# Kernel tuning notes

Hardware: AMD Instinct MI355X
Metric: run time of the kernel (lower is better)

Reference implementation:

```python
import jax, jax.numpy as jnp
import numpy as np

PAD_ID = 0


def setup_inputs() -> dict:
    key = jax.random.key(0)
    ks = jax.random.split(key, 12)
    B, T, A, E, H, V = 32, 512, 512, 256, 320, 8192
    s = 0.02
    emb = jax.random.normal(ks[0], (V, E), jnp.float32) * s
    emb = emb.at[PAD_ID].set(0.0)  # padding_idx row is zero
    return {
        "acoustic_tokens": jax.random.normal(ks[1], (B, T, A), jnp.float32),
        "decoder_inputs": jax.random.randint(ks[2], (B, T), 0, V),
        "emb": emb,
        "W_in": jax.random.normal(ks[3], (H, A + E), jnp.float32) * s,
        "b_in": jax.random.normal(ks[4], (H,), jnp.float32) * s,
        "W_ih": jax.random.normal(ks[5], (4 * H, H), jnp.float32) * s,
        "W_hh": jax.random.normal(ks[6], (4 * H, H), jnp.float32) * s,
        "b_ih": jax.random.normal(ks[7], (4 * H,), jnp.float32) * s,
        "b_hh": jax.random.normal(ks[8], (4 * H,), jnp.float32) * s,
        "W_out": jax.random.normal(ks[9], (V, H), jnp.float32) * s,
        "b_out": jax.random.normal(ks[10], (V,), jnp.float32) * s,
    }


def reference(acoustic_tokens, decoder_inputs, emb, W_in, b_in, W_ih, W_hh, b_ih, b_hh, W_out, b_out):
    B, T, A = acoustic_tokens.shape
    H = W_hh.shape[1]
    # zero pad row (padding_idx semantics)
    emb_m = emb * (jnp.arange(emb.shape[0]) != PAD_ID)[:, None].astype(emb.dtype)

    a_t = jnp.transpose(acoustic_tokens, (1, 0, 2))  # [T,B,A]
    tok_t = decoder_inputs.T                         # [T,B]

    def step(carry, xs):
        h, c = carry
        a, tok = xs
        e = emb_m[tok]                                           # [B,E]
        x = jnp.tanh(jnp.concatenate([a, e], -1) @ W_in.T + b_in)  # [B,H]
        gates = x @ W_ih.T + b_ih + h @ W_hh.T + b_hh            # [B,4H]
        i, f, g, o = jnp.split(gates, 4, axis=-1)
        c_new = jax.nn.sigmoid(f) * c + jax.nn.sigmoid(i) * jnp.tanh(g)
        h_new = jax.nn.sigmoid(o) * jnp.tanh(c_new)
        logits = h_new @ W_out.T + b_out  # dropout is identity in eval
        return (h_new, c_new), logits

    init = (jnp.zeros((B, H), acoustic_tokens.dtype), jnp.zeros((B, H), acoustic_tokens.dtype))
    _, logits = jax.lax.scan(step, init, (a_t, tok_t))  # [T,B,V]
    logits = jnp.transpose(logits, (1, 0, 2))           # [B,T,V]
    return jax.nn.log_softmax(logits, axis=-1)
```

## Files before the change

kernel.cpp:

```cpp
#include <hip/hip_runtime.h>
#include <hip/hip_bf16.h>

#define BB 32
#define TT 512
#define AA 512
#define EE 256
#define HH 320
#define VV 8192
#define KIN 768
#define G4 1280

#define NBLK 8
#define UPB 40
#define RTHR 640
#define GLP 161

#define POISON 0x7F7F7F7F7F7F7F7FULL

typedef __bf16 bf16x8v __attribute__((ext_vector_type(8)));
typedef float f32x4 __attribute__((ext_vector_type(4)));
typedef unsigned long long u64;

__device__ __forceinline__ float fsigm(float x) { return 1.f / (1.f + __expf(-x)); }
__device__ __forceinline__ float ftanh(float x) { return 2.f / (1.f + __expf(-2.f * x)) - 1.f; }
__device__ __forceinline__ unsigned short f2bf(float f) {
    __hip_bfloat16 h = __float2bfloat16(f);
    return *(unsigned short*)&h;
}

__global__ __launch_bounds__(320) void stage_x(const float* __restrict__ ac,
                                               const int* __restrict__ tok,
                                               const float* __restrict__ emb,
                                               const float* __restrict__ Win,
                                               const float* __restrict__ bin,
                                               float* __restrict__ X) {
    __shared__ float xs[8][KIN];
    const int r0 = blockIdx.x * 8;
    const int tid = threadIdx.x;
    for (int rr = 0; rr < 8; ++rr) {
        const int r = r0 + rr;
        const int t = r >> 5;
        const int b = r & 31;
        const int tk = tok[b * TT + t];
        const float4* ac4  = (const float4*)(ac + ((size_t)b * TT + t) * AA);
        const float4* emb4 = (const float4*)(emb + (size_t)tk * EE);
        float4* xs4 = (float4*)&xs[rr][0];
        for (int k4 = tid; k4 < KIN / 4; k4 += 320) {
            float4 v;
            if (k4 < AA / 4) v = ac4[k4];
            else if (tk == 0) v = make_float4(0.f, 0.f, 0.f, 0.f);
            else v = emb4[k4 - AA / 4];
            xs4[k4] = v;
        }
    }
    __syncthreads();
    const int j = tid;
    float acc[8];
    const float bj = bin[j];
#pragma unroll
    for (int rr = 0; rr < 8; ++rr) acc[rr] = bj;
    const float4* w4 = (const float4*)(Win + (size_t)j * KIN);
#pragma unroll 4
    for (int k4 = 0; k4 < KIN / 4; ++k4) {
        const float4 wv = w4[k4];
#pragma unroll
        for (int rr = 0; rr < 8; ++rr) {
            const float4 xv = ((const float4*)&xs[rr][0])[k4];
            acc[rr] += wv.x * xv.x + wv.y * xv.y + wv.z * xv.z + wv.w * xv.w;
        }
    }
#pragma unroll
    for (int rr = 0; rr < 8; ++rr)
        X[(size_t)(r0 + rr) * HH + j] = tanhf(acc[rr]);
}

__global__ __launch_bounds__(256) void stage_gin(const float* __restrict__ X,
                                                 const float* __restrict__ Wih,
                                                 const float* __restrict__ bih,
                                                 const float* __restrict__ bhh,
                                                 float* __restrict__ Gp) {
    __shared__ float xs[8][HH];
    const int r0 = blockIdx.x * 8;
    const int tid = threadIdx.x;
    {
        const float4* src = (const float4*)(X + (size_t)r0 * HH);
        float4* dst = (float4*)&xs[0][0];
        for (int k4 = tid; k4 < 8 * HH / 4; k4 += 256) dst[k4] = src[k4];
    }
    __syncthreads();
    const int t = r0 >> 5;
    const int b0 = r0 & 31;
    for (int p5 = 0; p5 < 5; ++p5) {
        const int j = tid + 256 * p5;
        const float bias = bih[j] + bhh[j];
        float acc[8];
#pragma unroll
        for (int rr = 0; rr < 8; ++rr) acc[rr] = bias;
        const float4* w4 = (const float4*)(Wih + (size_t)j * HH);
#pragma unroll 4
        for (int k4 = 0; k4 < HH / 4; ++k4) {
            const float4 wv = w4[k4];
#pragma unroll
            for (int rr = 0; rr < 8; ++rr) {
                const float4 xv = ((const float4*)&xs[rr][0])[k4];
                acc[rr] += wv.x * xv.x + wv.y * xv.y + wv.z * xv.z + wv.w * xv.w;
            }
        }
        const int q = j / HH;
        const int hi = j - q * HH;
        const int pp = hi / UPB;
        const int uu = hi - pp * UPB;
        const int ug = uu >> 2, u4 = uu & 3;
        float* dst = Gp + ((((size_t)t * NBLK + pp) * 4 + q) * 10 + ug) * 128 + u4;
#pragma unroll
        for (int rr = 0; rr < 8; ++rr) dst[(b0 + rr) * 4] = acc[rr];
    }
}

__global__ __launch_bounds__(256) void wcvt(const float* __restrict__ src,
                                            unsigned short* __restrict__ dst, int n4) {
    const int i = blockIdx.x * 256 + threadIdx.x;
    if (i < n4) {
        const float4 v = ((const float4*)src)[i];
        ushort4 o;
        o.x = f2bf(v.x); o.y = f2bf(v.y); o.z = f2bf(v.z); o.w = f2bf(v.w);
        ((ushort4*)dst)[i] = o;
    }
}

__global__ __launch_bounds__(256) void wcvt_whh(const float* __restrict__ Whh,
                                                unsigned short* __restrict__ dst) {
    const int i = blockIdx.x * 256 + threadIdx.x;
    if (i >= NBLK * 10 * 10 * 64) return;
    const int l = i & 63;
    const int kc = (i >> 6) % 10;
    const int tw = (i / 640) % 10;
    const int p = i / 6400;
    const int sr = tw * 16 + (l & 15);
    const int grow = (sr / UPB) * HH + p * UPB + (sr % UPB);
    const int k0 = kc * 32 + (l >> 4) * 8;
    const float* s = Whh + (size_t)grow * HH + k0;
    const float4 v0 = *(const float4*)s;
    const float4 v1 = *(const float4*)(s + 4);
    unsigned short tmp[8] = { f2bf(v0.x), f2bf(v0.y), f2bf(v0.z), f2bf(v0.w),
                              f2bf(v1.x), f2bf(v1.y), f2bf(v1.z), f2bf(v1.w) };
    *(uint4*)(dst + (size_t)i * 8) = *(const uint4*)tmp;
}

__global__ __launch_bounds__(RTHR) void stage_rec(const float* __restrict__ Gp,
                                                  const unsigned short* __restrict__ Whhp,
                                                  unsigned short* __restrict__ Hsb,
                                                  unsigned short* __restrict__ hb) {
    const int p = blockIdx.x;
    const int tid = threadIdx.x;
    const int l = tid & 63, w = tid >> 6;
    const int lr = l & 15, lk = l >> 4;

    __shared__ unsigned short Hl[32][328];
    __shared__ float Gl[BB * GLP];

    bf16x8v bfr[10];
#pragma unroll
    for (int kc = 0; kc < 10; ++kc)
        bfr[kc] = *(const bf16x8v*)(Whhp + ((size_t)((p * 10 + w) * 10 + kc) * 64 + l) * 8);

    const int mc = tid & 31;
    const int gidx = tid >> 5;
    const int uc0 = gidx * 4;
    float c0 = 0.f, c1 = 0.f, c2 = 0.f, c3 = 0.f;

    const int sm = tid / 20;
    const int sk = (tid - sm * 20) * 16;

    for (int t = 0; t < TT; ++t) {
        float4 g[4];
        if (gidx < 10) {
            const size_t gbase = ((size_t)t * NBLK + p) * 4;
#pragma unroll
            for (int q = 0; q < 4; ++q)
                g[q] = ((const float4*)Gp)[(gbase + q) * 320 + (size_t)gidx * 32 + mc];
        }
        if (t > 0) {
            const int slot = (t - 1) & 3;
            const u64* src = (const u64*)(hb + ((size_t)slot * BB + sm) * HH + sk);
            u64 v0, v1, v2, v3;
            for (;;) {
                v0 = __hip_atomic_load(src + 0, __ATOMIC_RELAXED, __HIP_MEMORY_SCOPE_AGENT);
                v1 = __hip_atomic_load(src + 1, __ATOMIC_RELAXED, __HIP_MEMORY_SCOPE_AGENT);
                v2 = __hip_atomic_load(src + 2, __ATOMIC_RELAXED, __HIP_MEMORY_SCOPE_AGENT);
                v3 = __hip_atomic_load(src + 3, __ATOMIC_RELAXED, __HIP_MEMORY_SCOPE_AGENT);
                if (v0 != POISON && v1 != POISON && v2 != POISON && v3 != POISON) break;
            }
            u64* d = (u64*)&Hl[sm][sk];
            d[0] = v0; d[1] = v1; d[2] = v2; d[3] = v3;
        }
        __syncthreads();
        if (t > 0) {
            f32x4 acc0 = {}, acc1 = {};
#pragma unroll
            for (int kc = 0; kc < 10; ++kc) {
                const bf16x8v av0 = *(const bf16x8v*)&Hl[lr][kc * 32 + lk * 8];
                const bf16x8v av1 = *(const bf16x8v*)&Hl[16 + lr][kc * 32 + lk * 8];
                acc0 = __builtin_amdgcn_mfma_f32_16x16x32_bf16(av0, bfr[kc], acc0, 0, 0, 0);
                acc1 = __builtin_amdgcn_mfma_f32_16x16x32_bf16(av1, bfr[kc], acc1, 0, 0, 0);
            }
#pragma unroll
            for (int rg = 0; rg < 4; ++rg) {
                Gl[(lk * 4 + rg) * GLP + w * 16 + lr] = acc0[rg];
                Gl[(16 + lk * 4 + rg) * GLP + w * 16 + lr] = acc1[rg];
            }
        }
        __syncthreads();

        if (gidx < 10) {
            float a[4][4];
#pragma unroll
            for (int q = 0; q < 4; ++q) {
                const float* gl = &Gl[mc * GLP + q * UPB + uc0];
                a[q][0] = g[q].x + (t > 0 ? gl[0] : 0.f);
                a[q][1] = g[q].y + (t > 0 ? gl[1] : 0.f);
                a[q][2] = g[q].z + (t > 0 ? gl[2] : 0.f);
                a[q][3] = g[q].w + (t > 0 ? gl[3] : 0.f);
            }
            const float n0 = fsigm(a[1][0]) * c0 + fsigm(a[0][0]) * ftanh(a[2][0]);
            const float n1 = fsigm(a[1][1]) * c1 + fsigm(a[0][1]) * ftanh(a[2][1]);
            const float n2 = fsigm(a[1][2]) * c2 + fsigm(a[0][2]) * ftanh(a[2][2]);
            const float n3 = fsigm(a[1][3]) * c3 + fsigm(a[0][3]) * ftanh(a[2][3]);
            const float h0 = fsigm(a[3][0]) * ftanh(n0);
            const float h1 = fsigm(a[3][1]) * ftanh(n1);
            const float h2 = fsigm(a[3][2]) * ftanh(n2);
            const float h3 = fsigm(a[3][3]) * ftanh(n3);
            c0 = n0; c1 = n1; c2 = n2; c3 = n3;
            const u64 hpk =
                (u64)f2bf(h0) | ((u64)f2bf(h1) << 16) |
                ((u64)f2bf(h2) << 32) | ((u64)f2bf(h3) << 48);
            *(u64*)(Hsb + ((size_t)mc * TT + t) * HH + p * UPB + uc0) = hpk;
            const size_t off = (size_t)mc * HH + p * UPB + uc0;
            __hip_atomic_store((u64*)(hb + ((size_t)(t & 3) * BB * HH) + off), hpk,
                               __ATOMIC_RELAXED, __HIP_MEMORY_SCOPE_AGENT);
            __hip_atomic_store((u64*)(hb + ((size_t)((t + 2) & 3) * BB * HH) + off), POISON,
                               __ATOMIC_RELAXED, __HIP_MEMORY_SCOPE_AGENT);
        }
    }
}

__global__ __launch_bounds__(256, 2) void stage_logits_mfma(const unsigned short* __restrict__ A,
                                                            const unsigned short* __restrict__ Bm,
                                                            const float* __restrict__ bout,
                                                            float* __restrict__ out) {
    __shared__ unsigned short As[128][40];
    __shared__ unsigned short Bs[128][40];
    const int tid = threadIdx.x;
    const int m0 = blockIdx.y * 128;
    const int n0 = blockIdx.x * 128;
    const int w = tid >> 6, l = tid & 63;
    const int wr = w >> 1, wc = w & 1;
    const int lr = l & 15, lk = l >> 4;

    f32x4 acc[4][4] = {};
    for (int k0 = 0; k0 < HH; k0 += 32) {
#pragma unroll
        for (int i = 0; i < 2; ++i) {
            const int uidx = tid + 256 * i;
            const int rr = uidx >> 2, ss = uidx & 3;
            *(uint4*)&As[rr][ss * 8] = *(const uint4*)(A + (size_t)(m0 + rr) * HH + k0 + ss * 8);
            *(uint4*)&Bs[rr][ss * 8] = *(const uint4*)(Bm + (size_t)(n0 + rr) * HH + k0 + ss * 8);
        }
        __syncthreads();
        bf16x8v af[4], bfr[4];
#pragma unroll
        for (int f = 0; f < 4; ++f) {
            af[f]  = *(const bf16x8v*)&As[wr * 64 + f * 16 + lr][lk * 8];
            bfr[f] = *(const bf16x8v*)&Bs[wc * 64 + f * 16 + lr][lk * 8];
        }
#pragma unroll
        for (int fm = 0; fm < 4; ++fm)
#pragma unroll
            for (int fn = 0; fn < 4; ++fn)
                acc[fm][fn] = __builtin_amdgcn_mfma_f32_16x16x32_bf16(af[fm], bfr[fn], acc[fm][fn], 0, 0, 0);
        __syncthreads();
    }
#pragma unroll
    for (int fn = 0; fn < 4; ++fn) {
        const int n = n0 + wc * 64 + fn * 16 + lr;
        const float bv = bout[n];
#pragma unroll
        for (int fm = 0; fm < 4; ++fm) {
            const int mbase = m0 + wr * 64 + fm * 16 + lk * 4;
#pragma unroll
            for (int rg = 0; rg < 4; ++rg)
                out[(size_t)(mbase + rg) * VV + n] = acc[fm][fn][rg] + bv;
        }
    }
}

__global__ __launch_bounds__(256) void stage_lsm(float* __restrict__ out) {
    __shared__ float buf[VV];
    __shared__ float red[16];
    const size_t m = blockIdx.x;
    float4* row4 = (float4*)(out + m * VV);
    float4* buf4 = (float4*)buf;
    const int tid = threadIdx.x;

    float mx = -INFINITY;
    for (int k4 = tid; k4 < VV / 4; k4 += 256) {
        const float4 v = row4[k4];
        buf4[k4] = v;
        mx = fmaxf(mx, fmaxf(fmaxf(v.x, v.y), fmaxf(v.z, v.w)));
    }
#pragma unroll
    for (int off = 32; off > 0; off >>= 1) mx = fmaxf(mx, __shfl_down(mx, off, 64));
    if ((tid & 63) == 0) red[tid >> 6] = mx;
    __syncthreads();
    if (tid == 0) {
        float m2 = red[0];
        for (int i = 1; i < 4; ++i) m2 = fmaxf(m2, red[i]);
        red[0] = m2;
    }
    __syncthreads();
    mx = red[0];

    float s = 0.f;
    for (int k4 = tid; k4 < VV / 4; k4 += 256) {
        const float4 v = buf4[k4];
        s += __expf(v.x - mx) + __expf(v.y - mx) + __expf(v.z - mx) + __expf(v.w - mx);
    }
#pragma unroll
    for (int off = 32; off > 0; off >>= 1) s += __shfl_down(s, off, 64);
    if ((tid & 63) == 0) red[8 + (tid >> 6)] = s;
    __syncthreads();
    if (tid == 0) {
        float s2 = 0.f;
        for (int i = 0; i < 4; ++i) s2 += red[8 + i];
        red[8] = logf(s2);
    }
    __syncthreads();
    const float lse = mx + red[8];
    for (int k4 = tid; k4 < VV / 4; k4 += 256) {
        float4 v = buf4[k4];
        v.x -= lse; v.y -= lse; v.z -= lse; v.w -= lse;
        row4[k4] = v;
    }
}

extern "C" void kernel_launch(void* const* d_in, const int* in_sizes, int n_in,
                              void* d_out, int out_size, void* d_ws, size_t ws_size,
                              hipStream_t stream) {
    const float* ac   = (const float*)d_in[0];
    const int*   tok  = (const int*)d_in[1];
    const float* emb  = (const float*)d_in[2];
    const float* Win  = (const float*)d_in[3];
    const float* bin  = (const float*)d_in[4];
    const float* Wih  = (const float*)d_in[5];
    const float* Whh  = (const float*)d_in[6];
    const float* bih  = (const float*)d_in[7];
    const float* bhh  = (const float*)d_in[8];
    const float* Wout = (const float*)d_in[9];
    const float* bout = (const float*)d_in[10];
    float* out = (float*)d_out;

    float* X  = (float*)d_ws;
    float* Gp = X + (size_t)TT * BB * HH;
    unsigned short* Hsb   = (unsigned short*)(Gp + (size_t)TT * BB * G4);
    unsigned short* Woutb = Hsb + (size_t)TT * BB * HH;
    unsigned short* Whhp  = Woutb + (size_t)VV * HH;
    unsigned short* hb    = Whhp + (size_t)NBLK * 10 * 10 * 64 * 8;

    stage_x<<<dim3(TT * BB / 8), dim3(320), 0, stream>>>(ac, tok, emb, Win, bin, X);
    stage_gin<<<dim3(TT * BB / 8), dim3(256), 0, stream>>>(X, Wih, bih, bhh, Gp);
    wcvt<<<dim3((VV * HH / 4 + 255) / 256), dim3(256), 0, stream>>>(Wout, Woutb, VV * HH / 4);
    wcvt_whh<<<dim3((NBLK * 10 * 10 * 64 + 255) / 256), dim3(256), 0, stream>>>(Whh, Whhp);
    hipMemsetAsync(hb, 0x7F, (size_t)4 * BB * HH * sizeof(unsigned short), stream);
    stage_rec<<<dim3(NBLK), dim3(RTHR), 0, stream>>>(Gp, Whhp, Hsb, hb);
    stage_logits_mfma<<<dim3(VV / 128, TT * BB / 128), dim3(256), 0, stream>>>(Hsb, Woutb, bout, out);
    stage_lsm<<<dim3(TT * BB), dim3(256), 0, stream>>>(out);
}
```

Baseline: 4.018 ms.

## Fuse LSTM cell into MFMA wavefronts via gate-interleaved layout and lane shuffles

The gate rows of W_hh and the precomputed input gates are permuted so each group of four adjacent MFMA output columns holds the i,f,g,o gates of one hidden unit. The cell update then runs directly on the MFMA accumulators, using lane shuffles instead of a shared-memory round trip and a second __syncthreads per timestep. The H staging buffer is double-buffered to avoid a write-after-read hazard, and the poison check switches to a per-16-bit zero test. The goal is a shorter serial critical path per step, at the cost of more shuffle and select arithmetic.

```diff
diff --git a/kernel.cpp b/kernel.cpp
--- a/kernel.cpp
+++ b/kernel.cpp
@@ -13,7 +13,6 @@
 #define NBLK 8
 #define UPB 40
 #define RTHR 640
-#define GLP 161
 
 #define POISON 0x7F7F7F7F7F7F7F7FULL
 
@@ -26,6 +25,19 @@
 __device__ __forceinline__ unsigned short f2bf(float f) {
     __hip_bfloat16 h = __float2bfloat16(f);
     return *(unsigned short*)&h;
+}
+__device__ __forceinline__ u64 zero16(u64 y) {
+    return (y - 0x0001000100010001ULL) & ~y & 0x8000800080008000ULL;
+}
+__device__ __forceinline__ float pick4(f32x4 v, int i) {
+    const float ab = (i & 1) ? v[1] : v[0];
+    const float cd = (i & 1) ? v[3] : v[2];
+    return (i & 2) ? cd : ab;
+}
+__device__ __forceinline__ float sel4(float a, float b, float c, float d, int i) {
+    const float ab = (i & 1) ? b : a;
+    const float cd = (i & 1) ? d : c;
+    return (i & 2) ? cd : ab;
 }
 
 __global__ __launch_bounds__(320) void stage_x(const float* __restrict__ ac,
@@ -109,11 +121,11 @@
         const int q = j / HH;
         const int hi = j - q * HH;
         const int pp = hi / UPB;
-        const int uu = hi - pp * UPB;
-        const int ug = uu >> 2, u4 = uu & 3;
-        float* dst = Gp + ((((size_t)t * NBLK + pp) * 4 + q) * 10 + ug) * 128 + u4;
-#pragma unroll
-        for (int rr = 0; rr < 8; ++rr) dst[(b0 + rr) * 4] = acc[rr];
+        const int lu = hi - pp * UPB;
+        const int rowp = lu * 4 + q;
+        float* dst = Gp + (((size_t)t * NBLK + pp) * 160 + rowp) * 32 + b0;
+#pragma unroll
+        for (int rr = 0; rr < 8; ++rr) dst[rr] = acc[rr];
     }
 }
 
@@ -137,7 +149,8 @@
     const int tw = (i / 640) % 10;
     const int p = i / 6400;
     const int sr = tw * 16 + (l & 15);
-    const int grow = (sr / UPB) * HH + p * UPB + (sr % UPB);
+    const int lu = sr >> 2, q = sr & 3;
+    const int grow = q * HH + p * UPB + lu;
     const int k0 = kc * 32 + (l >> 4) * 8;
     const float* s = Whh + (size_t)grow * HH + k0;
     const float4 v0 = *(const float4*)s;
@@ -155,31 +168,26 @@
     const int tid = threadIdx.x;
     const int l = tid & 63, w = tid >> 6;
     const int lr = l & 15, lk = l >> 4;
-
-    __shared__ unsigned short Hl[32][328];
-    __shared__ float Gl[BB * GLP];
+    const int q = lr & 3;
+    const int a = lr >> 2;
+
+    __shared__ unsigned short Hl[2][32][328];
 
     bf16x8v bfr[10];
 #pragma unroll
     for (int kc = 0; kc < 10; ++kc)
         bfr[kc] = *(const bf16x8v*)(Whhp + ((size_t)((p * 10 + w) * 10 + kc) * 64 + l) * 8);
 
-    const int mc = tid & 31;
-    const int gidx = tid >> 5;
-    const int uc0 = gidx * 4;
-    float c0 = 0.f, c1 = 0.f, c2 = 0.f, c3 = 0.f;
+    float c0 = 0.f, c1 = 0.f;
 
     const int sm = tid / 20;
     const int sk = (tid - sm * 20) * 16;
 
     for (int t = 0; t < TT; ++t) {
-        float4 g[4];
-        if (gidx < 10) {
-            const size_t gbase = ((size_t)t * NBLK + p) * 4;
-#pragma unroll
-            for (int q = 0; q < 4; ++q)
-                g[q] = ((const float4*)Gp)[(gbase + q) * 320 + (size_t)gidx * 32 + mc];
-        }
+        const float* gp = Gp + (((size_t)t * NBLK + p) * 160 + 16 * w + lr) * 32;
+        const float4 ga = *(const float4*)(gp + lk * 4);
+        const float4 gb = *(const float4*)(gp + 16 + lk * 4);
+
         if (t > 0) {
             const int slot = (t - 1) & 3;
             const u64* src = (const u64*)(hb + ((size_t)slot * BB + sm) * HH + sk);
@@ -189,57 +197,69 @@
                 v1 = __hip_atomic_load(src + 1, __ATOMIC_RELAXED, __HIP_MEMORY_SCOPE_AGENT);
                 v2 = __hip_atomic_load(src + 2, __ATOMIC_RELAXED, __HIP_MEMORY_SCOPE_AGENT);
                 v3 = __hip_atomic_load(src + 3, __ATOMIC_RELAXED, __HIP_MEMORY_SCOPE_AGENT);
-                if (v0 != POISON && v1 != POISON && v2 != POISON && v3 != POISON) break;
+                const u64 bad = zero16(v0 ^ POISON) | zero16(v1 ^ POISON) |
+                                zero16(v2 ^ POISON) | zero16(v3 ^ POISON);
+                if (bad == 0) break;
             }
-            u64* d = (u64*)&Hl[sm][sk];
+            u64* d = (u64*)&Hl[t & 1][sm][sk];
             d[0] = v0; d[1] = v1; d[2] = v2; d[3] = v3;
         }
         __syncthreads();
+
+        f32x4 acc0 = {}, acc1 = {};
         if (t > 0) {
-            f32x4 acc0 = {}, acc1 = {};
 #pragma unroll
             for (int kc = 0; kc < 10; ++kc) {
-                const bf16x8v av0 = *(const bf16x8v*)&Hl[lr][kc * 32 + lk * 8];
-                const bf16x8v av1 = *(const bf16x8v*)&Hl[16 + lr][kc * 32 + lk * 8];
+                const bf16x8v av0 = *(const bf16x8v*)&Hl[t & 1][lr][kc * 32 + lk * 8];
+                const bf16x8v av1 = *(const bf16x8v*)&Hl[t & 1][16 + lr][kc * 32 + lk * 8];
                 acc0 = __builtin_amdgcn_mfma_f32_16x16x32_bf16(av0, bfr[kc], acc0, 0, 0, 0);
                 acc1 = __builtin_amdgcn_mfma_f32_16x16x32_bf16(av1, bfr[kc], acc1, 0, 0, 0);
             }
-#pragma unroll
-            for (int rg = 0; rg < 4; ++rg) {
-                Gl[(lk * 4 + rg) * GLP + w * 16 + lr] = acc0[rg];
-                Gl[(16 + lk * 4 + rg) * GLP + w * 16 + lr] = acc1[rg];
-            }
-        }
-        __syncthreads();
-
-        if (gidx < 10) {
-            float a[4][4];
-#pragma unroll
-            for (int q = 0; q < 4; ++q) {
-                const float* gl = &Gl[mc * GLP + q * UPB + uc0];
-                a[q][0] = g[q].x + (t > 0 ? gl[0] : 0.f);
-                a[q][1] = g[q].y + (t > 0 ? gl[1] : 0.f);
-                a[q][2] = g[q].z + (t > 0 ? gl[2] : 0.f);
-                a[q][3] = g[q].w + (t > 0 ? gl[3] : 0.f);
-            }
-            const float n0 = fsigm(a[1][0]) * c0 + fsigm(a[0][0]) * ftanh(a[2][0]);
-            const float n1 = fsigm(a[1][1]) * c1 + fsigm(a[0][1]) * ftanh(a[2][1]);
-            const float n2 = fsigm(a[1][2]) * c2 + fsigm(a[0][2]) * ftanh(a[2][2]);
-            const float n3 = fsigm(a[1][3]) * c3 + fsigm(a[0][3]) * ftanh(a[2][3]);
-            const float h0 = fsigm(a[3][0]) * ftanh(n0);
-            const float h1 = fsigm(a[3][1]) * ftanh(n1);
-            const float h2 = fsigm(a[3][2]) * ftanh(n2);
-            const float h3 = fsigm(a[3][3]) * ftanh(n3);
-            c0 = n0; c1 = n1; c2 = n2; c3 = n3;
-            const u64 hpk =
-                (u64)f2bf(h0) | ((u64)f2bf(h1) << 16) |
-                ((u64)f2bf(h2) << 32) | ((u64)f2bf(h3) << 48);
-            *(u64*)(Hsb + ((size_t)mc * TT + t) * HH + p * UPB + uc0) = hpk;
-            const size_t off = (size_t)mc * HH + p * UPB + uc0;
-            __hip_atomic_store((u64*)(hb + ((size_t)(t & 3) * BB * HH) + off), hpk,
-                               __ATOMIC_RELAXED, __HIP_MEMORY_SCOPE_AGENT);
-            __hip_atomic_store((u64*)(hb + ((size_t)((t + 2) & 3) * BB * HH) + off), POISON,
-                               __ATOMIC_RELAXED, __HIP_MEMORY_SCOPE_AGENT);
+        }
+        f32x4 tot0 = acc0, tot1 = acc1;
+        tot0[0] += ga.x; tot0[1] += ga.y; tot0[2] += ga.z; tot0[3] += ga.w;
+        tot1[0] += gb.x; tot1[1] += gb.y; tot1[2] += gb.z; tot1[3] += gb.w;
+
+        const float s00 = pick4(tot0, q);
+        const float s01 = __shfl_xor(pick4(tot0, q ^ 1), 1, 64);
+        const float s02 = __shfl_xor(pick4(tot0, q ^ 2), 2, 64);
+        const float s03 = __shfl_xor(pick4(tot0, q ^ 3), 3, 64);
+        const float s10 = pick4(tot1, q);
+        const float s11 = __shfl_xor(pick4(tot1, q ^ 1), 1, 64);
+        const float s12 = __shfl_xor(pick4(tot1, q ^ 2), 2, 64);
+        const float s13 = __shfl_xor(pick4(tot1, q ^ 3), 3, 64);
+        const float gi0 = sel4(s00, s01, s02, s03, q);
+        const float gf0 = sel4(s00, s01, s02, s03, q ^ 1);
+        const float gg0 = sel4(s00, s01, s02, s03, q ^ 2);
+        const float go0 = sel4(s00, s01, s02, s03, q ^ 3);
+        const float gi1 = sel4(s10, s11, s12, s13, q);
+        const float gf1 = sel4(s10, s11, s12, s13, q ^ 1);
+        const float gg1 = sel4(s10, s11, s12, s13, q ^ 2);
+        const float go1 = sel4(s10, s11, s12, s13, q ^ 3);
+
+        const float cn0 = fsigm(gf0) * c0 + fsigm(gi0) * ftanh(gg0);
+        const float hn0 = fsigm(go0) * ftanh(cn0);
+        const float cn1 = fsigm(gf1) * c1 + fsigm(gi1) * ftanh(gg1);
+        const float hn1 = fsigm(go1) * ftanh(cn1);
+        c0 = cn0; c1 = cn1;
+
+        unsigned int x0 = f2bf(hn0), x1 = f2bf(hn1);
+        const unsigned int p0 = x0 | ((unsigned int)__shfl_xor((int)x0, 4, 64) << 16);
+        const unsigned int p1 = x1 | ((unsigned int)__shfl_xor((int)x1, 4, 64) << 16);
+        const u64 w0 = (u64)p0 | ((u64)(unsigned int)__shfl_xor((int)p0, 8, 64) << 32);
+        const u64 w1 = (u64)p1 | ((u64)(unsigned int)__shfl_xor((int)p1, 8, 64) << 32);
+        if (a == 0) {
+            const int b0 = lk * 4 + q;
+            const int ub = p * UPB + 4 * w;
+            *(u64*)(Hsb + ((size_t)b0 * TT + t) * HH + ub) = w0;
+            *(u64*)(Hsb + ((size_t)(b0 + 16) * TT + t) * HH + ub) = w1;
+            const size_t o0 = (size_t)b0 * HH + ub, o1 = (size_t)(b0 + 16) * HH + ub;
+            const size_t d_s = (size_t)(t & 3) * BB * HH;
+            const size_t p_s = (size_t)((t + 2) & 3) * BB * HH;
+            __hip_atomic_store((u64*)(hb + d_s + o0), w0, __ATOMIC_RELAXED, __HIP_MEMORY_SCOPE_AGENT);
+            __hip_atomic_store((u64*)(hb + d_s + o1), w1, __ATOMIC_RELAXED, __HIP_MEMORY_SCOPE_AGENT);
+            __hip_atomic_store((u64*)(hb + p_s + o0), POISON, __ATOMIC_RELAXED, __HIP_MEMORY_SCOPE_AGENT);
+            __hip_atomic_store((u64*)(hb + p_s + o1), POISON, __ATOMIC_RELAXED, __HIP_MEMORY_SCOPE_AGENT);
         }
     }
 }
```

New measurement: 4.772 ms. 18.8% more time.

## Move input projection and input-gate GEMMs to bf16 MFMA kernels

Applied to the files above, without the earlier changes.

Replaces the scalar fp32 stage_x and stage_gin kernels with tiled bf16 MFMA GEMMs. W_in and W_ih are first converted to bf16, the intermediate X buffer is stored in bf16, and the acoustic/embedding gather is folded into the A-tile load with on-the-fly bf16 conversion. The goal is to cut the time of these two precompute GEMMs, which used FMA loops with per-thread weight rows. In exchange, precision drops to bf16 for these products, and the Gp scatter stores are now less coalesced.

```diff
diff --git a/kernel.cpp b/kernel.cpp
--- a/kernel.cpp
+++ b/kernel.cpp
@@ -28,95 +28,6 @@
     return *(unsigned short*)&h;
 }
 
-__global__ __launch_bounds__(320) void stage_x(const float* __restrict__ ac,
-                                               const int* __restrict__ tok,
-                                               const float* __restrict__ emb,
-                                               const float* __restrict__ Win,
-                                               const float* __restrict__ bin,
-                                               float* __restrict__ X) {
-    __shared__ float xs[8][KIN];
-    const int r0 = blockIdx.x * 8;
-    const int tid = threadIdx.x;
-    for (int rr = 0; rr < 8; ++rr) {
-        const int r = r0 + rr;
-        const int t = r >> 5;
-        const int b = r & 31;
-        const int tk = tok[b * TT + t];
-        const float4* ac4  = (const float4*)(ac + ((size_t)b * TT + t) * AA);
-        const float4* emb4 = (const float4*)(emb + (size_t)tk * EE);
-        float4* xs4 = (float4*)&xs[rr][0];
-        for (int k4 = tid; k4 < KIN / 4; k4 += 320) {
-            float4 v;
-            if (k4 < AA / 4) v = ac4[k4];
-            else if (tk == 0) v = make_float4(0.f, 0.f, 0.f, 0.f);
-            else v = emb4[k4 - AA / 4];
-            xs4[k4] = v;
-        }
-    }
-    __syncthreads();
-    const int j = tid;
-    float acc[8];
-    const float bj = bin[j];
-#pragma unroll
-    for (int rr = 0; rr < 8; ++rr) acc[rr] = bj;
-    const float4* w4 = (const float4*)(Win + (size_t)j * KIN);
-#pragma unroll 4
-    for (int k4 = 0; k4 < KIN / 4; ++k4) {
-        const float4 wv = w4[k4];
-#pragma unroll
-        for (int rr = 0; rr < 8; ++rr) {
-            const float4 xv = ((const float4*)&xs[rr][0])[k4];
-            acc[rr] += wv.x * xv.x + wv.y * xv.y + wv.z * xv.z + wv.w * xv.w;
-        }
-    }
-#pragma unroll
-    for (int rr = 0; rr < 8; ++rr)
-        X[(size_t)(r0 + rr) * HH + j] = tanhf(acc[rr]);
-}
-
-__global__ __launch_bounds__(256) void stage_gin(const float* __restrict__ X,
-                                                 const float* __restrict__ Wih,
-                                                 const float* __restrict__ bih,
-                                                 const float* __restrict__ bhh,
-                                                 float* __restrict__ Gp) {
-    __shared__ float xs[8][HH];
-    const int r0 = blockIdx.x * 8;
-    const int tid = threadIdx.x;
-    {
-        const float4* src = (const float4*)(X + (size_t)r0 * HH);
-        float4* dst = (float4*)&xs[0][0];
-        for (int k4 = tid; k4 < 8 * HH / 4; k4 += 256) dst[k4] = src[k4];
-    }
-    __syncthreads();
-    const int t = r0 >> 5;
-    const int b0 = r0 & 31;
-    for (int p5 = 0; p5 < 5; ++p5) {
-        const int j = tid + 256 * p5;
-        const float bias = bih[j] + bhh[j];
-        float acc[8];
-#pragma unroll
-        for (int rr = 0; rr < 8; ++rr) acc[rr] = bias;
-        const float4* w4 = (const float4*)(Wih + (size_t)j * HH);
-#pragma unroll 4
-        for (int k4 = 0; k4 < HH / 4; ++k4) {
-            const float4 wv = w4[k4];
-#pragma unroll
-            for (int rr = 0; rr < 8; ++rr) {
-                const float4 xv = ((const float4*)&xs[rr][0])[k4];
-                acc[rr] += wv.x * xv.x + wv.y * xv.y + wv.z * xv.z + wv.w * xv.w;
-            }
-        }
-        const int q = j / HH;
-        const int hi = j - q * HH;
-        const int pp = hi / UPB;
-        const int uu = hi - pp * UPB;
-        const int ug = uu >> 2, u4 = uu & 3;
-        float* dst = Gp + ((((size_t)t * NBLK + pp) * 4 + q) * 10 + ug) * 128 + u4;
-#pragma unroll
-        for (int rr = 0; rr < 8; ++rr) dst[(b0 + rr) * 4] = acc[rr];
-    }
-}
-
 __global__ __launch_bounds__(256) void wcvt(const float* __restrict__ src,
                                             unsigned short* __restrict__ dst, int n4) {
     const int i = blockIdx.x * 256 + threadIdx.x;
@@ -125,6 +36,142 @@
         ushort4 o;
         o.x = f2bf(v.x); o.y = f2bf(v.y); o.z = f2bf(v.z); o.w = f2bf(v.w);
         ((ushort4*)dst)[i] = o;
+    }
+}
+
+__global__ __launch_bounds__(256, 2) void stage_x_mfma(const float* __restrict__ ac,
+                                                       const int* __restrict__ tok,
+                                                       const float* __restrict__ emb,
+                                                       const unsigned short* __restrict__ Winb,
+                                                       const float* __restrict__ bin,
+                                                       unsigned short* __restrict__ Xb) {
+    __shared__ unsigned short As[128][40];
+    __shared__ unsigned short Bs[64][40];
+    const int tid = threadIdx.x;
+    const int m0 = blockIdx.y * 128;
+    const int n0 = blockIdx.x * 64;
+    const int w = tid >> 6, l = tid & 63;
+    const int wr = w >> 1, wc = w & 1;
+    const int lr = l & 15, lk = l >> 4;
+
+    f32x4 acc[4][2] = {};
+    for (int k0 = 0; k0 < KIN; k0 += 32) {
+        {
+            const int rr = tid >> 1;
+            const int c0 = (tid & 1) * 16;
+            const int m = m0 + rr;
+            const int t = m >> 5, b = m & 31;
+            const int k = k0 + c0;
+            float tmp[16];
+            if (k < AA) {
+                const float4* s = (const float4*)(ac + ((size_t)b * TT + t) * AA + k);
+#pragma unroll
+                for (int e = 0; e < 4; ++e) *(float4*)&tmp[4 * e] = s[e];
+            } else {
+                const int tk = tok[b * TT + t];
+                if (tk == 0) {
+#pragma unroll
+                    for (int e = 0; e < 16; ++e) tmp[e] = 0.f;
+                } else {
+                    const float4* s = (const float4*)(emb + (size_t)tk * EE + (k - AA));
+#pragma unroll
+                    for (int e = 0; e < 4; ++e) *(float4*)&tmp[4 * e] = s[e];
+                }
+            }
+            unsigned short o[16];
+#pragma unroll
+            for (int e = 0; e < 16; ++e) o[e] = f2bf(tmp[e]);
+            *(uint4*)&As[rr][c0] = *(const uint4*)&o[0];
+            *(uint4*)&As[rr][c0 + 8] = *(const uint4*)&o[8];
+        }
+        {
+            const int rr = tid >> 2, ss = tid & 3;
+            *(uint4*)&Bs[rr][ss * 8] = *(const uint4*)(Winb + (size_t)(n0 + rr) * KIN + k0 + ss * 8);
+        }
+        __syncthreads();
+        bf16x8v af[4], bfv[2];
+#pragma unroll
+        for (int f = 0; f < 4; ++f) af[f] = *(const bf16x8v*)&As[wr * 64 + f * 16 + lr][lk * 8];
+#pragma unroll
+        for (int g = 0; g < 2; ++g) bfv[g] = *(const bf16x8v*)&Bs[wc * 32 + g * 16 + lr][lk * 8];
+#pragma unroll
+        for (int f = 0; f < 4; ++f)
+#pragma unroll
+            for (int g = 0; g < 2; ++g)
+                acc[f][g] = __builtin_amdgcn_mfma_f32_16x16x32_bf16(af[f], bfv[g], acc[f][g], 0, 0, 0);
+        __syncthreads();
+    }
+#pragma unroll
+    for (int g = 0; g < 2; ++g) {
+        const int n = n0 + wc * 32 + g * 16 + lr;
+        const float bv = bin[n];
+#pragma unroll
+        for (int f = 0; f < 4; ++f) {
+            const int mbase = m0 + wr * 64 + f * 16 + lk * 4;
+#pragma unroll
+            for (int rg = 0; rg < 4; ++rg)
+                Xb[(size_t)(mbase + rg) * HH + n] = f2bf(tanhf(acc[f][g][rg] + bv));
+        }
+    }
+}
+
+__global__ __launch_bounds__(256, 2) void stage_gin_mfma(const unsigned short* __restrict__ A,
+                                                         const unsigned short* __restrict__ Bm,
+                                                         const float* __restrict__ bih,
+                                                         const float* __restrict__ bhh,
+                                                         float* __restrict__ Gp) {
+    __shared__ unsigned short As[128][40];
+    __shared__ unsigned short Bs[128][40];
+    const int tid = threadIdx.x;
+    const int m0 = blockIdx.y * 128;
+    const int n0 = blockIdx.x * 128;
+    const int w = tid >> 6, l = tid & 63;
+    const int wr = w >> 1, wc = w & 1;
+    const int lr = l & 15, lk = l >> 4;
+
+    f32x4 acc[4][4] = {};
+    for (int k0 = 0; k0 < HH; k0 += 32) {
+#pragma unroll
+        for (int i = 0; i < 2; ++i) {
+            const int uidx = tid + 256 * i;
+            const int rr = uidx >> 2, ss = uidx & 3;
+            *(uint4*)&As[rr][ss * 8] = *(const uint4*)(A + (size_t)(m0 + rr) * HH + k0 + ss * 8);
+            *(uint4*)&Bs[rr][ss * 8] = *(const uint4*)(Bm + (size_t)(n0 + rr) * HH + k0 + ss * 8);
+        }
+        __syncthreads();
+        bf16x8v af[4], bfv[4];
+#pragma unroll
+        for (int f = 0; f < 4; ++f) {
+            af[f]  = *(const bf16x8v*)&As[wr * 64 + f * 16 + lr][lk * 8];
+            bfv[f] = *(const bf16x8v*)&Bs[wc * 64 + f * 16 + lr][lk * 8];
+        }
+#pragma unroll
+        for (int fm = 0; fm < 4; ++fm)
+#pragma unroll
+            for (int fn = 0; fn < 4; ++fn)
+                acc[fm][fn] = __builtin_amdgcn_mfma_f32_16x16x32_bf16(af[fm], bfv[fn], acc[fm][fn], 0, 0, 0);
+        __syncthreads();
+    }
+#pragma unroll
+    for (int fn = 0; fn < 4; ++fn) {
+        const int j = n0 + wc * 64 + fn * 16 + lr;
+        const float bias = bih[j] + bhh[j];
+        const int q = j / HH;
+        const int hi = j - q * HH;
+        const int pp = hi / UPB;
+        const int uu = hi - pp * UPB;
+        const int ug = uu >> 2, u4 = uu & 3;
+#pragma unroll
+        for (int fm = 0; fm < 4; ++fm) {
+            const int mbase = m0 + wr * 64 + fm * 16 + lk * 4;
+#pragma unroll
+            for (int rg = 0; rg < 4; ++rg) {
+                const int m = mbase + rg;
+                const int t = m >> 5, b = m & 31;
+                Gp[((((size_t)t * NBLK + pp) * 4 + q) * 10 + ug) * 128 + b * 4 + u4] =
+                    acc[fm][fn][rg] + bias;
+            }
+        }
     }
 }
 
@@ -267,17 +314,17 @@
             *(uint4*)&Bs[rr][ss * 8] = *(const uint4*)(Bm + (size_t)(n0 + rr) * HH + k0 + ss * 8);
         }
         __syncthreads();
-        bf16x8v af[4], bfr[4];
+        bf16x8v af[4], bfv[4];
 #pragma unroll
         for (int f = 0; f < 4; ++f) {
             af[f]  = *(const bf16x8v*)&As[wr * 64 + f * 16 + lr][lk * 8];
-            bfr[f] = *(const bf16x8v*)&Bs[wc * 64 + f * 16 + lr][lk * 8];
+            bfv[f] = *(const bf16x8v*)&Bs[wc * 64 + f * 16 + lr][lk * 8];
         }
 #pragma unroll
         for (int fm = 0; fm < 4; ++fm)
 #pragma unroll
             for (int fn = 0; fn < 4; ++fn)
-                acc[fm][fn] = __builtin_amdgcn_mfma_f32_16x16x32_bf16(af[fm], bfr[fn], acc[fm][fn], 0, 0, 0);
+                acc[fm][fn] = __builtin_amdgcn_mfma_f32_16x16x32_bf16(af[fm], bfv[fn], acc[fm][fn], 0, 0, 0);
         __syncthreads();
     }
 #pragma unroll
@@ -359,17 +406,21 @@
     const float* bout = (const float*)d_in[10];
     float* out = (float*)d_out;
 
-    float* X  = (float*)d_ws;
-    float* Gp = X + (size_t)TT * BB * HH;
-    unsigned short* Hsb   = (unsigned short*)(Gp + (size_t)TT * BB * G4);
+    float* Gp = (float*)d_ws;
+    unsigned short* Xb    = (unsigned short*)(Gp + (size_t)TT * BB * G4);
+    unsigned short* Hsb   = Xb + (size_t)TT * BB * HH;
     unsigned short* Woutb = Hsb + (size_t)TT * BB * HH;
-    unsigned short* Whhp  = Woutb + (size_t)VV * HH;
+    unsigned short* Winb  = Woutb + (size_t)VV * HH;
+    unsigned short* Wihb  = Winb + (size_t)HH * KIN;
+    unsigned short* Whhp  = Wihb + (size_t)G4 * HH;
     unsigned short* hb    = Whhp + (size_t)NBLK * 10 * 10 * 64 * 8;
 
-    stage_x<<<dim3(TT * BB / 8), dim3(320), 0, stream>>>(ac, tok, emb, Win, bin, X);
-    stage_gin<<<dim3(TT * BB / 8), dim3(256), 0, stream>>>(X, Wih, bih, bhh, Gp);
+    wcvt<<<dim3((HH * KIN / 4 + 255) / 256), dim3(256), 0, stream>>>(Win, Winb, HH * KIN / 4);
+    wcvt<<<dim3((G4 * HH / 4 + 255) / 256), dim3(256), 0, stream>>>(Wih, Wihb, G4 * HH / 4);
     wcvt<<<dim3((VV * HH / 4 + 255) / 256), dim3(256), 0, stream>>>(Wout, Woutb, VV * HH / 4);
     wcvt_whh<<<dim3((NBLK * 10 * 10 * 64 + 255) / 256), dim3(256), 0, stream>>>(Whh, Whhp);
+    stage_x_mfma<<<dim3(HH / 64, TT * BB / 128), dim3(256), 0, stream>>>(ac, tok, emb, Winb, bin, Xb);
+    stage_gin_mfma<<<dim3(G4 / 128, TT * BB / 128), dim3(256), 0, stream>>>(Xb, Wihb, bih, bhh, Gp);
     hipMemsetAsync(hb, 0x7F, (size_t)4 * BB * HH * sizeof(unsigned short), stream);
     stage_rec<<<dim3(NBLK), dim3(RTHR), 0, stream>>>(Gp, Whhp, Hsb, hb);
     stage_logits_mfma<<<dim3(VV / 128, TT * BB / 128), dim3(256), 0, stream>>>(Hsb, Woutb, bout, out);
```

Result: faster. 3.291 ms (-18.1%).
